# Optimization experiments

Hardware: AMD Instinct MI355X
Metric: run time of the kernel (lower is better)

The kernel has to match this reference:

```python
import jax, jax.numpy as jnp
import numpy as np

N_NODES = 50000
N_EDGES = 800000
NODE_DIM = 256
EDGE_DIM = 64
NUM_REL = 4
HID = 512      # hidden_dims[0]
LAST = 128     # last_dim_size
BATCH = 16384
EPS = 1e-10    # torchdrug RelationalGraphConv degree-normalization eps


def _glorot(k, shape):
    fan_in = shape[-1]
    return jax.random.normal(k, shape, jnp.float32) / np.sqrt(fan_in).astype(np.float32)


def setup_inputs() -> dict:
    key = jax.random.key(0)
    ks = jax.random.split(key, 20)
    inp = {}
    inp["inputs"] = jax.random.randint(ks[0], (BATCH, 3), 0, N_NODES, dtype=jnp.int32)
    inp["node_feature"] = jax.random.normal(ks[1], (N_NODES, NODE_DIM), jnp.float32)
    inp["edge_feature"] = jax.random.normal(ks[2], (N_EDGES, EDGE_DIM), jnp.float32)
    inp["edge_src"] = jax.random.randint(ks[3], (N_EDGES,), 0, N_NODES, dtype=jnp.int32)
    inp["edge_dst"] = jax.random.randint(ks[4], (N_EDGES,), 0, N_NODES, dtype=jnp.int32)
    inp["edge_rel"] = jax.random.randint(ks[5], (N_EDGES,), 0, NUM_REL, dtype=jnp.int32)
    # RGCN layer 1: 256 -> 512
    inp["We1"] = _glorot(ks[6], (NODE_DIM, EDGE_DIM)); inp["be1"] = jnp.zeros((NODE_DIM,), jnp.float32)
    inp["Wl1"] = _glorot(ks[7], (HID, NUM_REL * NODE_DIM)); inp["bl1"] = jnp.zeros((HID,), jnp.float32)
    inp["Ws1"] = _glorot(ks[8], (HID, NODE_DIM)); inp["bs1"] = jnp.zeros((HID,), jnp.float32)
    # RGCN layer 2: 512 -> 128
    inp["We2"] = _glorot(ks[9], (HID, EDGE_DIM)); inp["be2"] = jnp.zeros((HID,), jnp.float32)
    inp["Wl2"] = _glorot(ks[10], (LAST, NUM_REL * HID)); inp["bl2"] = jnp.zeros((LAST,), jnp.float32)
    inp["Ws2"] = _glorot(ks[11], (LAST, HID)); inp["bs2"] = jnp.zeros((LAST,), jnp.float32)
    # ccle_mlp: edge_dim -> 256 -> 128
    inp["Wc1"] = _glorot(ks[12], (256, EDGE_DIM)); inp["bc1"] = jnp.zeros((256,), jnp.float32)
    inp["Wc2"] = _glorot(ks[13], (LAST, 256)); inp["bc2"] = jnp.zeros((LAST,), jnp.float32)
    # final MLP: 3*128 -> 128 -> 64 -> 1
    inp["Wf1"] = _glorot(ks[14], (128, 3 * LAST)); inp["bf1"] = jnp.zeros((128,), jnp.float32)
    inp["Wf2"] = _glorot(ks[15], (64, 128)); inp["bf2"] = jnp.zeros((64,), jnp.float32)
    inp["Wf3"] = _glorot(ks[16], (1, 64)); inp["bf3"] = jnp.zeros((1,), jnp.float32)
    return inp


def _rgcn_layer(x, edge_src, edge_dst, edge_rel, edge_feat, We, be, Wl, bl, Ws, bs):
    """torchdrug RelationalGraphConv: message = x[src] + edge_linear(edge_feat);
    per-(node,relation) mean aggregation; combine = linear(update) + self_loop(x); relu."""
    in_dim = x.shape[1]
    msg = x[edge_src] + edge_feat @ We.T + be                      # [E, in_dim]
    seg = edge_dst * NUM_REL + edge_rel                            # [E]
    agg = jax.ops.segment_sum(msg, seg, num_segments=N_NODES * NUM_REL)
    cnt = jax.ops.segment_sum(jnp.ones((msg.shape[0], 1), msg.dtype), seg,
                              num_segments=N_NODES * NUM_REL)
    upd = (agg / (cnt + EPS)).reshape(N_NODES, NUM_REL * in_dim)   # [N, R*in_dim]
    return jax.nn.relu(upd @ Wl.T + bl + x @ Ws.T + bs)


def reference(inputs, node_feature, edge_feature, edge_src, edge_dst, edge_rel,
              We1, be1, Wl1, bl1, Ws1, bs1,
              We2, be2, Wl2, bl2, Ws2, bs2,
              Wc1, bc1, Wc2, bc2,
              Wf1, bf1, Wf2, bf2, Wf3, bf3):
    d1, d2, ctx = inputs[:, 0], inputs[:, 1], inputs[:, 2]
    h = _rgcn_layer(node_feature, edge_src, edge_dst, edge_rel, edge_feature,
                    We1, be1, Wl1, bl1, Ws1, bs1)
    h = _rgcn_layer(h, edge_src, edge_dst, edge_rel, edge_feature,
                    We2, be2, Wl2, bl2, Ws2, bs2)
    x1 = h[d1]                                                     # [B, 128]
    x2 = h[d2]                                                     # [B, 128]
    ef = edge_feature[ctx]                                         # [B, 64]
    x3 = jax.nn.relu(ef @ Wc1.T + bc1) @ Wc2.T + bc2               # [B, 128]
    x = jnp.concatenate([x1, x2, x3], axis=1)                      # [B, 384]
    x = jax.nn.relu(x @ Wf1.T + bf1)
    x = jax.nn.relu(x @ Wf2.T + bf2)
    return x @ Wf3.T + bf3                                         # [B, 1]
```

## Files before the change

### kernel.cpp

```cpp
#include <hip/hip_runtime.h>
#include <hip/hip_bf16.h>

#define N_NODES 50000
#define N_EDGES 800000
#define NODE_DIM 256
#define EDGE_DIM 64
#define NUM_REL 4
#define HID 512
#define LAST 128
#define BATCH 16384
#define EPS 1e-10f
#define NSEG (N_NODES * NUM_REL)

#define K1 1600
#define K2 832

typedef __bf16 bf16_t;
typedef __attribute__((ext_vector_type(8))) __bf16 bf16x8;
typedef __attribute__((ext_vector_type(4))) __bf16 bf16x4;
typedef __attribute__((ext_vector_type(2))) __bf16 bf16x2;
typedef __attribute__((ext_vector_type(4))) float f32x4;

typedef __attribute__((address_space(1))) const unsigned int g_u32;
typedef __attribute__((address_space(3))) unsigned int l_u32;
static __device__ __forceinline__ void gload16(const void* g, void* l) {
    __builtin_amdgcn_global_load_lds((g_u32*)g, (l_u32*)l, 16, 0, 0);
}

__global__ __launch_bounds__(256) void hist_kernel(
    const int* __restrict__ edst, const int* __restrict__ erel, int* __restrict__ hist)
{
    int e = blockIdx.x * 256 + threadIdx.x;
    if (e >= N_EDGES) return;
    atomicAdd(&hist[edst[e] * NUM_REL + erel[e]], 1);
}

#define SCAN_B 2048
__global__ __launch_bounds__(256) void scan1(
    const int* __restrict__ in, int* __restrict__ out, int* __restrict__ bsum, int n)
{
    __shared__ int sh[256];
    int base = blockIdx.x * SCAN_B + threadIdx.x * 8;
    int v[8]; int s = 0;
#pragma unroll
    for (int i = 0; i < 8; ++i) {
        int idx = base + i;
        v[i] = s;
        s += (idx < n) ? in[idx] : 0;
    }
    sh[threadIdx.x] = s;
    __syncthreads();
    for (int off = 1; off < 256; off <<= 1) {
        int t = (threadIdx.x >= off) ? sh[threadIdx.x - off] : 0;
        __syncthreads();
        sh[threadIdx.x] += t;
        __syncthreads();
    }
    int texcl = (threadIdx.x == 0) ? 0 : sh[threadIdx.x - 1];
#pragma unroll
    for (int i = 0; i < 8; ++i) {
        int idx = base + i;
        if (idx < n) out[idx] = texcl + v[i];
    }
    if (threadIdx.x == 255) bsum[blockIdx.x] = sh[255];
}

__global__ void scan2(int* bsum, int nb)
{
    if (threadIdx.x == 0 && blockIdx.x == 0) {
        int s = 0;
        for (int i = 0; i < nb; ++i) { int t = bsum[i]; bsum[i] = s; s += t; }
    }
}

__global__ __launch_bounds__(256) void scan3(int* __restrict__ out, const int* __restrict__ bsum, int n)
{
    int idx = blockIdx.x * SCAN_B + threadIdx.x * 8;
    int add = bsum[blockIdx.x];
#pragma unroll
    for (int i = 0; i < 8; ++i)
        if (idx + i < n) out[idx + i] += add;
}

__global__ __launch_bounds__(256) void csr_fill(
    const int* __restrict__ edst, const int* __restrict__ erel, const int* __restrict__ esrc,
    const int* __restrict__ offs, int* __restrict__ cursor,
    int* __restrict__ csr_src, int* __restrict__ csr_eid)
{
    int e = blockIdx.x * 256 + threadIdx.x;
    if (e >= N_EDGES) return;
    int seg = edst[e] * NUM_REL + erel[e];
    int pos = offs[seg] + atomicAdd(&cursor[seg], 1);
    csr_src[pos] = esrc[e];
    csr_eid[pos] = e;
}

__global__ __launch_bounds__(256) void prep_small(
    const float* __restrict__ Wc1, const float* __restrict__ Wc2,
    const float* __restrict__ Wf1, const float* __restrict__ Wf2,
    const float* __restrict__ bl1, const float* __restrict__ bs1,
    const float* __restrict__ bl2, const float* __restrict__ bs2,
    bf16_t* __restrict__ Wc1b, bf16_t* __restrict__ Wc2b,
    bf16_t* __restrict__ Wf1b, bf16_t* __restrict__ Wf2b,
    float* __restrict__ bias12, float* __restrict__ bias22)
{
    int i = blockIdx.x * 256 + threadIdx.x;
    const float* src; bf16_t* dst; int base;
    if (i < 4096)        { src = Wc1; dst = Wc1b; base = 0; }
    else if (i < 12288)  { src = Wc2; dst = Wc2b; base = 4096; }
    else if (i < 24576)  { src = Wf1; dst = Wf1b; base = 12288; }
    else if (i < 26624)  { src = Wf2; dst = Wf2b; base = 24576; }
    else {
        int j = i - 26624;
        if (j < 512) bias12[j] = bl1[j] + bs1[j];
        else if (j < 640) bias22[j - 512] = bl2[j - 512] + bs2[j - 512];
        return;
    }
    int k = i - base;
    float4 v = ((const float4*)src)[k];
    bf16x4 o;
    o[0] = (bf16_t)v.x; o[1] = (bf16_t)v.y; o[2] = (bf16_t)v.z; o[3] = (bf16_t)v.w;
    ((bf16x4*)dst)[k] = o;
}

__global__ __launch_bounds__(256) void xconv_k(const float* __restrict__ x, bf16_t* __restrict__ A1,
                                               bf16_t* __restrict__ xb)
{
    int i = blockIdx.x * 256 + threadIdx.x;
    int n = i >> 6;
    int c4 = i & 63;
    float4 v = ((const float4*)(x + (size_t)n * 256))[c4];
    bf16x4 o;
    o[0] = (bf16_t)v.x; o[1] = (bf16_t)v.y; o[2] = (bf16_t)v.z; o[3] = (bf16_t)v.w;
    *(bf16x4*)(A1 + (size_t)n * K1 + 1280 + c4 * 4) = o;
    *(bf16x4*)(xb + (size_t)n * 256 + c4 * 4) = o;
}

__global__ __launch_bounds__(256) void prep_w1cat(
    const float* __restrict__ Wl1, const float* __restrict__ We1,
    const float* __restrict__ Ws1, const float* __restrict__ be1, bf16_t* __restrict__ W1cat)
{
    int j = blockIdx.x;
    int t = threadIdx.x;
    const float* wrow = Wl1 + (size_t)j * 1024;
    bf16_t* out = W1cat + (size_t)j * K1;
    for (int c = t; c < 1024; c += 256) out[c] = (bf16_t)wrow[c];
    {
        int r = t >> 6, e = t & 63;
        float s = 0.f;
        const float* wr = wrow + r * 256;
        for (int c = 0; c < 256; ++c) s += wr[c] * We1[c * 64 + e];
        out[1024 + t] = (bf16_t)s;
    }
    if (t < 256) out[1280 + t] = (bf16_t)Ws1[(size_t)j * 256 + t];
    if (t < 4) {
        float s = 0.f;
        const float* wr = wrow + t * 256;
        for (int c = 0; c < 256; ++c) s += wr[c] * be1[c];
        out[1536 + t] = (bf16_t)s;
    }
    if (t >= 4 && t < 64) out[1536 + t] = (bf16_t)0.f;
}

__global__ __launch_bounds__(256) void prep_w2cat(
    const float* __restrict__ Wl2, const float* __restrict__ We2,
    const float* __restrict__ Ws2, const float* __restrict__ be2, bf16_t* __restrict__ W2cat)
{
    int j = blockIdx.x;
    int t = threadIdx.x;
    const float* wrow = Wl2 + (size_t)j * 2048;
    bf16_t* out = W2cat + (size_t)j * K2;
    {
        int r = t >> 6, e = t & 63;
        float s = 0.f;
        const float* wr = wrow + r * 512;
        for (int k = 0; k < 512; ++k) s += wr[k] * We2[k * 64 + e];
        out[t] = (bf16_t)s;
    }
    for (int c = t; c < 512; c += 256) out[256 + c] = (bf16_t)Ws2[(size_t)j * 512 + c];
    if (t < 4) {
        float s = 0.f;
        const float* wr = wrow + t * 512;
        for (int k = 0; k < 512; ++k) s += wr[k] * be2[k];
        out[768 + t] = (bf16_t)s;
    }
    if (t >= 4 && t < 64) out[768 + t] = (bf16_t)0.f;
}

__global__ __launch_bounds__(256) void prep_w2p(const float* __restrict__ Wl2, bf16_t* __restrict__ W2p)
{
    int idx = blockIdx.x * 256 + threadIdx.x;
    int row = idx >> 9, k = idx & 511;
    int j = row & 127, r = row >> 7;
    W2p[idx] = (bf16_t)Wl2[(size_t)j * 2048 + r * 512 + k];
}

__global__ __launch_bounds__(256) void agg1(
    const float* __restrict__ ef, const bf16_t* __restrict__ xb,
    const int* __restrict__ csr_src, const int* __restrict__ csr_eid,
    const int* __restrict__ offs, const int* __restrict__ hist,
    bf16_t* __restrict__ A1, bf16_t* __restrict__ A2)
{
    int n = blockIdx.x;
    int w = threadIdx.x >> 6;
    int lane = threadIdx.x & 63;
    int half = lane >> 5;
    int l32 = lane & 31;
    int seg = n * NUM_REL + w;
    int beg = offs[seg], ct = hist[seg];

    float xs[8] = {0.f, 0.f, 0.f, 0.f, 0.f, 0.f, 0.f, 0.f};
    float es0 = 0.f, es1 = 0.f;

    int i = 0;
    for (; i + 4 <= ct; i += 4) {
        int sA = csr_src[beg + i + half];
        int sB = csr_src[beg + i + 2 + half];
        int eA = csr_eid[beg + i + half];
        int eB = csr_eid[beg + i + 2 + half];
        bf16x8 vA = *(const bf16x8*)(xb + (size_t)sA * 256 + l32 * 8);
        bf16x8 vB = *(const bf16x8*)(xb + (size_t)sB * 256 + l32 * 8);
        float2 fA = *(const float2*)(ef + (size_t)eA * 64 + l32 * 2);
        float2 fB = *(const float2*)(ef + (size_t)eB * 64 + l32 * 2);
#pragma unroll
        for (int j = 0; j < 8; ++j) xs[j] += (float)vA[j] + (float)vB[j];
        es0 += fA.x + fB.x;
        es1 += fA.y + fB.y;
    }
    for (; i + 2 <= ct; i += 2) {
        int sA = csr_src[beg + i + half];
        int eA = csr_eid[beg + i + half];
        bf16x8 vA = *(const bf16x8*)(xb + (size_t)sA * 256 + l32 * 8);
        float2 fA = *(const float2*)(ef + (size_t)eA * 64 + l32 * 2);
#pragma unroll
        for (int j = 0; j < 8; ++j) xs[j] += (float)vA[j];
        es0 += fA.x;
        es1 += fA.y;
    }
    if (i < ct && half == 0) {
        int sA = csr_src[beg + i];
        int eA = csr_eid[beg + i];
        bf16x8 vA = *(const bf16x8*)(xb + (size_t)sA * 256 + l32 * 8);
        float2 fA = *(const float2*)(ef + (size_t)eA * 64 + l32 * 2);
#pragma unroll
        for (int j = 0; j < 8; ++j) xs[j] += (float)vA[j];
        es0 += fA.x;
        es1 += fA.y;
    }
#pragma unroll
    for (int j = 0; j < 8; ++j) xs[j] += __shfl_xor(xs[j], 32);
    es0 += __shfl_xor(es0, 32);
    es1 += __shfl_xor(es1, 32);

    float inv = 1.0f / ((float)ct + EPS);
    if (half == 0) {
        bf16x8 m;
#pragma unroll
        for (int j = 0; j < 8; ++j) m[j] = (bf16_t)(xs[j] * inv);
        *(bf16x8*)(A1 + (size_t)n * K1 + w * 256 + l32 * 8) = m;
        bf16x2 e2;
        e2[0] = (bf16_t)(es0 * inv);
        e2[1] = (bf16_t)(es1 * inv);
        *(bf16x2*)(A1 + (size_t)n * K1 + 1024 + w * 64 + l32 * 2) = e2;
        *(bf16x2*)(A2 + (size_t)n * K2 + w * 64 + l32 * 2) = e2;
    }
    if (lane == 0) {
        bf16_t fv = (bf16_t)((float)ct * inv);
        A1[(size_t)n * K1 + 1536 + w] = fv;
        A2[(size_t)n * K2 + 768 + w] = fv;
    }
    if (w == 3 && lane >= 4) {
        A1[(size_t)n * K1 + 1536 + lane] = (bf16_t)0.f;
        A2[(size_t)n * K2 + 768 + lane] = (bf16_t)0.f;
    }
}

__global__ __launch_bounds__(256) void agg2(
    const bf16_t* __restrict__ P, const int* __restrict__ csr_src,
    const int* __restrict__ offs, const int* __restrict__ hist,
    float* __restrict__ h2base)
{
    __shared__ float red[4][128];
    int n = blockIdx.x;
    int w = threadIdx.x >> 6;
    int lane = threadIdx.x & 63;
    int half = lane >> 5;
    int l32 = lane & 31;
    int seg = n * NUM_REL + w;
    int beg = offs[seg], ct = hist[seg];

    float s0 = 0.f, s1 = 0.f, s2 = 0.f, s3 = 0.f;
    int i = 0;
    for (; i + 4 <= ct; i += 4) {
        int a = csr_src[beg + i + half];
        int b = csr_src[beg + i + 2 + half];
        bf16x4 va = *(const bf16x4*)(P + (size_t)a * HID + w * 128 + l32 * 4);
        bf16x4 vb = *(const bf16x4*)(P + (size_t)b * HID + w * 128 + l32 * 4);
        s0 += (float)va[0] + (float)vb[0];
        s1 += (float)va[1] + (float)vb[1];
        s2 += (float)va[2] + (float)vb[2];
        s3 += (float)va[3] + (float)vb[3];
    }
    for (; i + 2 <= ct; i += 2) {
        int a = csr_src[beg + i + half];
        bf16x4 va = *(const bf16x4*)(P + (size_t)a * HID + w * 128 + l32 * 4);
        s0 += (float)va[0]; s1 += (float)va[1]; s2 += (float)va[2]; s3 += (float)va[3];
    }
    if (i < ct && half == 0) {
        int a = csr_src[beg + i];
        bf16x4 va = *(const bf16x4*)(P + (size_t)a * HID + w * 128 + l32 * 4);
        s0 += (float)va[0]; s1 += (float)va[1]; s2 += (float)va[2]; s3 += (float)va[3];
    }
    s0 += __shfl_xor(s0, 32);
    s1 += __shfl_xor(s1, 32);
    s2 += __shfl_xor(s2, 32);
    s3 += __shfl_xor(s3, 32);

    float inv = 1.0f / ((float)ct + EPS);
    if (half == 0) {
        red[w][l32 * 4 + 0] = s0 * inv;
        red[w][l32 * 4 + 1] = s1 * inv;
        red[w][l32 * 4 + 2] = s2 * inv;
        red[w][l32 * 4 + 3] = s3 * inv;
    }
    __syncthreads();
    int t = threadIdx.x;
    if (t < 128)
        h2base[(size_t)n * 128 + t] = red[0][t] + red[1][t] + red[2][t] + red[3][t];
}

template<int RELU, int ACC, int OUTBF>
__global__ __launch_bounds__(256) void gemm_bf16(
    const bf16_t* __restrict__ A, int lda,
    const bf16_t* __restrict__ W, int ldw,
    const float* __restrict__ Cin, int ldcin,
    const float* __restrict__ bias,
    void* __restrict__ Cout, int ldc,
    int M, int N, int K, int ncol)
{
    __shared__ char smem[65536];
    const int tid = threadIdx.x;

    const int nwg = gridDim.x;
    const int q8 = nwg >> 3, r8 = nwg & 7;
    const int xcd = blockIdx.x & 7, li = blockIdx.x >> 3;
    const int wgid = (xcd < r8 ? xcd * (q8 + 1) : r8 * (q8 + 1) + (xcd - r8) * q8) + li;

    const int row0 = (wgid / ncol) * 128;
    const int col0 = (wgid % ncol) * 128;
    const int lane = tid & 63, wv = tid >> 6;

    const int rsub = lane >> 3;
    const int gchunk = (lane & 7) ^ rsub;
    const bf16_t* pa[4]; const bf16_t* pb[4];
    int lofs[4];
#pragma unroll
    for (int s = 0; s < 4; ++s) {
        int q = wv * 4 + s;
        int ar = row0 + q * 8 + rsub; if (ar >= M) ar = M - 1;
        int br = col0 + q * 8 + rsub; if (br >= N) br = N - 1;
        pa[s] = A + (size_t)ar * lda + gchunk * 8;
        pb[s] = W + (size_t)br * ldw + gchunk * 8;
        lofs[s] = q * 1024;
    }

    const int wm = wv >> 1, wn = wv & 1;
    const int r16 = lane & 15, kch = lane >> 4;
    const int sw = r16 & 7;

    f32x4 acc[4][4];
#pragma unroll
    for (int i = 0; i < 4; ++i)
#pragma unroll
        for (int j = 0; j < 4; ++j) acc[i][j] = (f32x4){0.f, 0.f, 0.f, 0.f};

#pragma unroll
    for (int s = 0; s < 4; ++s) {
        gload16(pa[s], smem + lofs[s]);
        gload16(pb[s], smem + 16384 + lofs[s]);
    }

    const int nk = K >> 6;
    int cur = 0;
    for (int it = 0; it < nk; ++it) {
        const int k0 = it << 6;
        if (it + 1 < nk) {
            char* nb = smem + ((cur ^ 1) << 15);
#pragma unroll
            for (int s = 0; s < 4; ++s) {
                gload16(pa[s] + k0 + 64, nb + lofs[s]);
                gload16(pb[s] + k0 + 64, nb + 16384 + lofs[s]);
            }
            asm volatile("s_waitcnt vmcnt(8)" ::: "memory");
        } else {
            asm volatile("s_waitcnt vmcnt(0)" ::: "memory");
        }
        __builtin_amdgcn_s_barrier();
        __builtin_amdgcn_sched_barrier(0);
        const char* As = smem + (cur << 15);
        const char* Bs = As + 16384;
#pragma unroll
        for (int t = 0; t < 2; ++t) {
            const int slot = ((t * 4 + kch) ^ sw) << 4;
            bf16x8 af[4], bfm[4];
#pragma unroll
            for (int i = 0; i < 4; ++i)
                af[i] = *(const bf16x8*)(As + (wm * 64 + i * 16 + r16) * 128 + slot);
#pragma unroll
            for (int j = 0; j < 4; ++j)
                bfm[j] = *(const bf16x8*)(Bs + (wn * 64 + j * 16 + r16) * 128 + slot);
#pragma unroll
            for (int i = 0; i < 4; ++i)
#pragma unroll
                for (int j = 0; j < 4; ++j)
                    acc[i][j] = __builtin_amdgcn_mfma_f32_16x16x32_bf16(af[i], bfm[j], acc[i][j], 0, 0, 0);
        }
        __builtin_amdgcn_s_barrier();
        cur ^= 1;
    }

    const int crow0 = row0 + wm * 64;
#pragma unroll
    for (int i = 0; i < 4; ++i) {
#pragma unroll
        for (int j = 0; j < 4; ++j) {
            int col = col0 + wn * 64 + j * 16 + r16;
            if (col >= N) continue;
            float bv = bias ? bias[col] : 0.f;
#pragma unroll
            for (int q = 0; q < 4; ++q) {
                int row = crow0 + i * 16 + kch * 4 + q;
                if (row >= M) continue;
                float v = acc[i][j][q] + bv;
                if (ACC) v += Cin[(size_t)row * ldcin + col];
                if (RELU) v = fmaxf(v, 0.f);
                if (OUTBF) ((bf16_t*)Cout)[(size_t)row * ldc + col] = (bf16_t)v;
                else       ((float*)Cout)[(size_t)row * ldc + col] = v;
            }
        }
    }
}

__global__ __launch_bounds__(256) void gather_head(
    const int* __restrict__ inputs, const bf16_t* __restrict__ h2,
    const float* __restrict__ ef, bf16_t* __restrict__ xcat, bf16_t* __restrict__ ef_g)
{
    int i = blockIdx.x;
    int t = threadIdx.x;
    int d1 = inputs[i * 3 + 0];
    int d2 = inputs[i * 3 + 1];
    int ctx = inputs[i * 3 + 2];
    if (t < 128) {
        xcat[(size_t)i * 384 + t] = h2[(size_t)d1 * LAST + t];
    } else {
        int c = t - 128;
        xcat[(size_t)i * 384 + 128 + c] = h2[(size_t)d2 * LAST + c];
    }
    if (t < 64) ef_g[(size_t)i * 64 + t] = (bf16_t)ef[(size_t)ctx * EDGE_DIM + t];
}

__global__ __launch_bounds__(256) void final_matvec(
    const bf16_t* __restrict__ f2, const float* __restrict__ Wf3,
    const float* __restrict__ bf3, float* __restrict__ out, int M)
{
    int row = blockIdx.x * 4 + (threadIdx.x >> 6);
    int lane = threadIdx.x & 63;
    if (row >= M) return;
    float v = (float)f2[(size_t)row * 64 + lane] * Wf3[lane];
#pragma unroll
    for (int off = 32; off > 0; off >>= 1) v += __shfl_down(v, off);
    if (lane == 0) out[row] = v + bf3[0];
}

extern "C" void kernel_launch(void* const* d_in, const int* in_sizes, int n_in,
                              void* d_out, int out_size, void* d_ws, size_t ws_size,
                              hipStream_t stream)
{
    const int*   inputs       = (const int*)  d_in[0];
    const float* node_feature = (const float*)d_in[1];
    const float* edge_feature = (const float*)d_in[2];
    const int*   edge_src     = (const int*)  d_in[3];
    const int*   edge_dst     = (const int*)  d_in[4];
    const int*   edge_rel     = (const int*)  d_in[5];
    const float* We1 = (const float*)d_in[6];
    const float* be1 = (const float*)d_in[7];
    const float* Wl1 = (const float*)d_in[8];
    const float* bl1 = (const float*)d_in[9];
    const float* Ws1 = (const float*)d_in[10];
    const float* bs1 = (const float*)d_in[11];
    const float* We2 = (const float*)d_in[12];
    const float* be2 = (const float*)d_in[13];
    const float* Wl2 = (const float*)d_in[14];
    const float* bl2 = (const float*)d_in[15];
    const float* Ws2 = (const float*)d_in[16];
    const float* bs2 = (const float*)d_in[17];
    const float* Wc1 = (const float*)d_in[18];
    const float* bc1 = (const float*)d_in[19];
    const float* Wc2 = (const float*)d_in[20];
    const float* bc2 = (const float*)d_in[21];
    const float* Wf1 = (const float*)d_in[22];
    const float* bf1 = (const float*)d_in[23];
    const float* Wf2 = (const float*)d_in[24];
    const float* bf2 = (const float*)d_in[25];
    const float* Wf3 = (const float*)d_in[26];
    const float* bf3 = (const float*)d_in[27];
    float* out = (float*)d_out;

    char* p = (char*)d_ws;
    auto alloc = [&](size_t bytes) { char* r = p; p += (bytes + 255) & ~(size_t)255; return r; };
    int* hist     = (int*)alloc(NSEG * 4);
    int* offs     = (int*)alloc(NSEG * 4);
    int* cursor   = (int*)alloc(NSEG * 4);
    int* csr_src  = (int*)alloc(N_EDGES * 4);
    int* csr_eid  = (int*)alloc(N_EDGES * 4);
    int* bsums    = (int*)alloc(128 * 4);
    bf16_t* A1    = (bf16_t*)alloc((size_t)N_NODES * K1 * 2);
    bf16_t* A2    = (bf16_t*)alloc((size_t)N_NODES * K2 * 2);
    bf16_t* xb    = (bf16_t*)alloc((size_t)N_NODES * 256 * 2);
    bf16_t* Pbuf  = (bf16_t*)alloc((size_t)N_NODES * HID * 2);
    float*  h2base= (float*)alloc((size_t)N_NODES * 128 * 4);
    bf16_t* h2    = (bf16_t*)alloc((size_t)N_NODES * 128 * 2);
    bf16_t* W1cat = (bf16_t*)alloc((size_t)512 * K1 * 2);
    bf16_t* W2cat = (bf16_t*)alloc((size_t)128 * K2 * 2);
    bf16_t* W2p   = (bf16_t*)alloc((size_t)512 * 512 * 2);
    bf16_t* Wc1b  = (bf16_t*)alloc(256 * 64 * 2);
    bf16_t* Wc2b  = (bf16_t*)alloc(128 * 256 * 2);
    bf16_t* Wf1b  = (bf16_t*)alloc(128 * 384 * 2);
    bf16_t* Wf2b  = (bf16_t*)alloc(64 * 128 * 2);
    float*  bias12= (float*)alloc(512 * 4);
    float*  bias22= (float*)alloc(128 * 4);
    bf16_t* ef_g  = (bf16_t*)alloc((size_t)BATCH * 64 * 2);
    bf16_t* u3    = (bf16_t*)alloc((size_t)BATCH * 256 * 2);
    bf16_t* xcat  = (bf16_t*)alloc((size_t)BATCH * 384 * 2);
    bf16_t* f1    = (bf16_t*)alloc((size_t)BATCH * 128 * 2);
    bf16_t* f2    = (bf16_t*)alloc((size_t)BATCH * 64 * 2);

    hipMemsetAsync(hist, 0, NSEG * 4, stream);
    hipMemsetAsync(cursor, 0, NSEG * 4, stream);
    hist_kernel<<<(N_EDGES + 255) / 256, 256, 0, stream>>>(edge_dst, edge_rel, hist);
    int nscan = (NSEG + SCAN_B - 1) / SCAN_B;
    scan1<<<nscan, 256, 0, stream>>>(hist, offs, bsums, NSEG);
    scan2<<<1, 64, 0, stream>>>(bsums, nscan);
    scan3<<<nscan, 256, 0, stream>>>(offs, bsums, NSEG);
    csr_fill<<<(N_EDGES + 255) / 256, 256, 0, stream>>>(edge_dst, edge_rel, edge_src,
                                                        offs, cursor, csr_src, csr_eid);

    prep_w1cat<<<512, 256, 0, stream>>>(Wl1, We1, Ws1, be1, W1cat);
    prep_w2cat<<<128, 256, 0, stream>>>(Wl2, We2, Ws2, be2, W2cat);
    prep_w2p<<<(512 * 512) / 256, 256, 0, stream>>>(Wl2, W2p);
    prep_small<<<(26624 + 640 + 255) / 256, 256, 0, stream>>>(
        Wc1, Wc2, Wf1, Wf2, bl1, bs1, bl2, bs2,
        Wc1b, Wc2b, Wf1b, Wf2b, bias12, bias22);
    xconv_k<<<(N_NODES * 64 + 255) / 256, 256, 0, stream>>>(node_feature, A1, xb);

    agg1<<<N_NODES, 256, 0, stream>>>(edge_feature, xb, csr_src, csr_eid, offs, hist, A1, A2);
    {
        int nrow = (N_NODES + 127) / 128, ncol = HID / 128;
        gemm_bf16<1, 0, 1><<<nrow * ncol, 256, 0, stream>>>(A1, K1, W1cat, K1, nullptr, 0, bias12,
                                                            A2 + 256, K2, N_NODES, HID, K1, ncol);
    }

    {
        int nrow = (N_NODES + 127) / 128, ncol = HID / 128;
        gemm_bf16<0, 0, 1><<<nrow * ncol, 256, 0, stream>>>(A2 + 256, K2, W2p, 512, nullptr, 0, nullptr,
                                                            Pbuf, HID, N_NODES, HID, 512, ncol);
    }
    agg2<<<N_NODES, 256, 0, stream>>>(Pbuf, csr_src, offs, hist, h2base);
    {
        int nrow = (N_NODES + 127) / 128;
        gemm_bf16<1, 1, 1><<<nrow, 256, 0, stream>>>(A2, K2, W2cat, K2, h2base, 128, bias22,
                                                     h2, 128, N_NODES, 128, K2, 1);
    }

    gather_head<<<BATCH, 256, 0, stream>>>(inputs, h2, edge_feature, xcat, ef_g);
    {
        gemm_bf16<1, 0, 1><<<(BATCH / 128) * 2, 256, 0, stream>>>(ef_g, 64, Wc1b, 64, nullptr, 0, bc1,
                                                                  u3, 256, BATCH, 256, 64, 2);
    }
    {
        gemm_bf16<0, 0, 1><<<BATCH / 128, 256, 0, stream>>>(u3, 256, Wc2b, 256, nullptr, 0, bc2,
                                                            xcat + 256, 384, BATCH, 128, 256, 1);
    }
    {
        gemm_bf16<1, 0, 1><<<BATCH / 128, 256, 0, stream>>>(xcat, 384, Wf1b, 384, nullptr, 0, bf1,
                                                            f1, 128, BATCH, 128, 384, 1);
    }
    {
        gemm_bf16<1, 0, 1><<<BATCH / 128, 256, 0, stream>>>(f1, 128, Wf2b, 128, nullptr, 0, bf2,
                                                            f2, 64, BATCH, 64, 128, 1);
    }
    final_matvec<<<BATCH / 4, 256, 0, stream>>>(f2, Wf3, bf3, out, BATCH);
}
```

Baseline: 705.5 us.

## Fuse head gathers into Wf1 GEMM, fuse Wf2+final matvec, drop cursor memset

The h2[d1]/h2[d2] gathers now happen inside a dedicated Wf1 GEMM kernel that loads rows by index straight into shared memory, so the concatenated xcat buffer is no longer materialized. The Wf2 GEMM and the final dot product are merged into one head_tail kernel. The edge-feature gather is vectorized. The scan also seeds the CSR cursor with offsets, which removes a memset and one load per edge in csr_fill. Together these cut launches and intermediate traffic in the small head stages, which are a minor share of total runtime.

```diff
diff --git a/kernel.cpp b/kernel.cpp
--- a/kernel.cpp
+++ b/kernel.cpp
@@ -73,24 +73,29 @@
     }
 }
 
-__global__ __launch_bounds__(256) void scan3(int* __restrict__ out, const int* __restrict__ bsum, int n)
+__global__ __launch_bounds__(256) void scan3(int* __restrict__ out, int* __restrict__ cursor,
+                                             const int* __restrict__ bsum, int n)
 {
     int idx = blockIdx.x * SCAN_B + threadIdx.x * 8;
     int add = bsum[blockIdx.x];
 #pragma unroll
     for (int i = 0; i < 8; ++i)
-        if (idx + i < n) out[idx + i] += add;
+        if (idx + i < n) {
+            int v = out[idx + i] + add;
+            out[idx + i] = v;
+            cursor[idx + i] = v;
+        }
 }
 
 __global__ __launch_bounds__(256) void csr_fill(
     const int* __restrict__ edst, const int* __restrict__ erel, const int* __restrict__ esrc,
-    const int* __restrict__ offs, int* __restrict__ cursor,
+    int* __restrict__ cursor,
     int* __restrict__ csr_src, int* __restrict__ csr_eid)
 {
     int e = blockIdx.x * 256 + threadIdx.x;
     if (e >= N_EDGES) return;
     int seg = edst[e] * NUM_REL + erel[e];
-    int pos = offs[seg] + atomicAdd(&cursor[seg], 1);
+    int pos = atomicAdd(&cursor[seg], 1);
     csr_src[pos] = esrc[e];
     csr_eid[pos] = e;
 }
@@ -441,35 +446,159 @@
     }
 }
 
-__global__ __launch_bounds__(256) void gather_head(
+__global__ __launch_bounds__(256) void gemm_f1g(
     const int* __restrict__ inputs, const bf16_t* __restrict__ h2,
-    const float* __restrict__ ef, bf16_t* __restrict__ xcat, bf16_t* __restrict__ ef_g)
-{
-    int i = blockIdx.x;
-    int t = threadIdx.x;
-    int d1 = inputs[i * 3 + 0];
-    int d2 = inputs[i * 3 + 1];
-    int ctx = inputs[i * 3 + 2];
-    if (t < 128) {
-        xcat[(size_t)i * 384 + t] = h2[(size_t)d1 * LAST + t];
-    } else {
-        int c = t - 128;
-        xcat[(size_t)i * 384 + 128 + c] = h2[(size_t)d2 * LAST + c];
-    }
-    if (t < 64) ef_g[(size_t)i * 64 + t] = (bf16_t)ef[(size_t)ctx * EDGE_DIM + t];
-}
-
-__global__ __launch_bounds__(256) void final_matvec(
-    const bf16_t* __restrict__ f2, const float* __restrict__ Wf3,
-    const float* __restrict__ bf3, float* __restrict__ out, int M)
-{
-    int row = blockIdx.x * 4 + (threadIdx.x >> 6);
-    int lane = threadIdx.x & 63;
-    if (row >= M) return;
-    float v = (float)f2[(size_t)row * 64 + lane] * Wf3[lane];
-#pragma unroll
-    for (int off = 32; off > 0; off >>= 1) v += __shfl_down(v, off);
-    if (lane == 0) out[row] = v + bf3[0];
+    const bf16_t* __restrict__ x3, const bf16_t* __restrict__ Wf1b,
+    const float* __restrict__ bf1, bf16_t* __restrict__ f1)
+{
+    __shared__ char smem[65536];
+    const int tid = threadIdx.x;
+    const int nwg = gridDim.x;
+    const int q8 = nwg >> 3;
+    const int xcd = blockIdx.x & 7, li = blockIdx.x >> 3;
+    const int wgid = xcd * q8 + li;
+    const int row0 = wgid * 128;
+    const int lane = tid & 63, wv = tid >> 6;
+
+    const int rsub = lane >> 3;
+    const int gchunk = (lane & 7) ^ rsub;
+    const bf16_t* baseA[4][3];
+    const bf16_t* pb[4];
+    int lofs[4];
+#pragma unroll
+    for (int s = 0; s < 4; ++s) {
+        int q = wv * 4 + s;
+        int ar = row0 + q * 8 + rsub;
+        int d1 = inputs[ar * 3 + 0];
+        int d2 = inputs[ar * 3 + 1];
+        baseA[s][0] = h2 + (size_t)d1 * 128 + gchunk * 8;
+        baseA[s][1] = h2 + (size_t)d2 * 128 + gchunk * 8;
+        baseA[s][2] = x3 + (size_t)ar * 128 + gchunk * 8;
+        int br = q * 8 + rsub;
+        pb[s] = Wf1b + (size_t)br * 384 + gchunk * 8;
+        lofs[s] = q * 1024;
+    }
+
+    const int wm = wv >> 1, wn = wv & 1;
+    const int r16 = lane & 15, kch = lane >> 4;
+    const int sw = r16 & 7;
+
+    f32x4 acc[4][4];
+#pragma unroll
+    for (int i = 0; i < 4; ++i)
+#pragma unroll
+        for (int j = 0; j < 4; ++j) acc[i][j] = (f32x4){0.f, 0.f, 0.f, 0.f};
+
+#pragma unroll
+    for (int s = 0; s < 4; ++s) {
+        gload16(baseA[s][0], smem + lofs[s]);
+        gload16(pb[s], smem + 16384 + lofs[s]);
+    }
+
+    int cur = 0;
+#pragma unroll
+    for (int it = 0; it < 6; ++it) {
+        const int k0 = it << 6;
+        if (it < 5) {
+            const int kn = k0 + 64;
+            const int reg = kn >> 7, off = kn & 127;
+            char* nb = smem + ((cur ^ 1) << 15);
+#pragma unroll
+            for (int s = 0; s < 4; ++s) {
+                gload16(baseA[s][reg] + off, nb + lofs[s]);
+                gload16(pb[s] + kn, nb + 16384 + lofs[s]);
+            }
+            asm volatile("s_waitcnt vmcnt(8)" ::: "memory");
+        } else {
+            asm volatile("s_waitcnt vmcnt(0)" ::: "memory");
+        }
+        __builtin_amdgcn_s_barrier();
+        __builtin_amdgcn_sched_barrier(0);
+        const char* As = smem + (cur << 15);
+        const char* Bs = As + 16384;
+#pragma unroll
+        for (int t = 0; t < 2; ++t) {
+            const int slot = ((t * 4 + kch) ^ sw) << 4;
+            bf16x8 af[4], bfm[4];
+#pragma unroll
+            for (int i = 0; i < 4; ++i)
+                af[i] = *(const bf16x8*)(As + (wm * 64 + i * 16 + r16) * 128 + slot);
+#pragma unroll
+            for (int j = 0; j < 4; ++j)
+                bfm[j] = *(const bf16x8*)(Bs + (wn * 64 + j * 16 + r16) * 128 + slot);
+#pragma unroll
+            for (int i = 0; i < 4; ++i)
+#pragma unroll
+                for (int j = 0; j < 4; ++j)
+                    acc[i][j] = __builtin_amdgcn_mfma_f32_16x16x32_bf16(af[i], bfm[j], acc[i][j], 0, 0, 0);
+        }
+        __builtin_amdgcn_s_barrier();
+        cur ^= 1;
+    }
+
+    const int crow0 = row0 + wm * 64;
+#pragma unroll
+    for (int i = 0; i < 4; ++i) {
+#pragma unroll
+        for (int j = 0; j < 4; ++j) {
+            int col = wn * 64 + j * 16 + r16;
+            if (col >= 128) continue;
+            float bv = bf1[col];
+#pragma unroll
+            for (int q = 0; q < 4; ++q) {
+                int row = crow0 + i * 16 + kch * 4 + q;
+                float v = fmaxf(acc[i][j][q] + bv, 0.f);
+                f1[(size_t)row * 128 + col] = (bf16_t)v;
+            }
+        }
+    }
+}
+
+__global__ __launch_bounds__(256) void gather_ef(
+    const int* __restrict__ inputs, const float* __restrict__ ef, bf16_t* __restrict__ ef_g)
+{
+    int i = blockIdx.x * 256 + threadIdx.x;
+    int row = i >> 4, c4 = i & 15;
+    int ctx = inputs[row * 3 + 2];
+    float4 v = *(const float4*)(ef + (size_t)ctx * 64 + c4 * 4);
+    bf16x4 o;
+    o[0] = (bf16_t)v.x; o[1] = (bf16_t)v.y; o[2] = (bf16_t)v.z; o[3] = (bf16_t)v.w;
+    *(bf16x4*)(ef_g + (size_t)row * 64 + c4 * 4) = o;
+}
+
+__global__ __launch_bounds__(256) void head_tail(
+    const bf16_t* __restrict__ f1, const bf16_t* __restrict__ Wf2b,
+    const float* __restrict__ bf2, const float* __restrict__ Wf3,
+    const float* __restrict__ bf3, float* __restrict__ out)
+{
+    __shared__ bf16_t sf1[128 * 128];
+    int blk = blockIdx.x;
+    int tid = threadIdx.x;
+    const bf16_t* gsrc = f1 + (size_t)blk * 128 * 128;
+    for (int i = tid; i < 128 * 16; i += 256)
+        ((bf16x8*)sf1)[i] = ((const bf16x8*)gsrc)[i];
+    int lane = tid & 63, wv = tid >> 6;
+    bf16x8 w[16];
+#pragma unroll
+    for (int c = 0; c < 16; ++c) w[c] = ((const bf16x8*)(Wf2b + lane * 128))[c];
+    float bias2 = bf2[lane];
+    float wf3 = Wf3[lane];
+    float b3 = bf3[0];
+    __syncthreads();
+    for (int r = wv; r < 128; r += 4) {
+        const bf16x8* frow = (const bf16x8*)(sf1 + r * 128);
+        float acc = 0.f;
+#pragma unroll
+        for (int c = 0; c < 16; ++c) {
+            bf16x8 fv = frow[c];
+#pragma unroll
+            for (int j = 0; j < 8; ++j) acc += (float)fv[j] * (float)w[c][j];
+        }
+        float v = fmaxf(acc + bias2, 0.f) * wf3;
+#pragma unroll
+        for (int off = 32; off > 0; off >>= 1) v += __shfl_down(v, off);
+        if (lane == 0) out[blk * 128 + r] = v + b3;
+    }
 }
 
 extern "C" void kernel_launch(void* const* d_in, const int* in_sizes, int n_in,
@@ -531,19 +660,17 @@
     float*  bias22= (float*)alloc(128 * 4);
     bf16_t* ef_g  = (bf16_t*)alloc((size_t)BATCH * 64 * 2);
     bf16_t* u3    = (bf16_t*)alloc((size_t)BATCH * 256 * 2);
-    bf16_t* xcat  = (bf16_t*)alloc((size_t)BATCH * 384 * 2);
+    bf16_t* x3buf = (bf16_t*)alloc((size_t)BATCH * 128 * 2);
     bf16_t* f1    = (bf16_t*)alloc((size_t)BATCH * 128 * 2);
-    bf16_t* f2    = (bf16_t*)alloc((size_t)BATCH * 64 * 2);
 
     hipMemsetAsync(hist, 0, NSEG * 4, stream);
-    hipMemsetAsync(cursor, 0, NSEG * 4, stream);
     hist_kernel<<<(N_EDGES + 255) / 256, 256, 0, stream>>>(edge_dst, edge_rel, hist);
     int nscan = (NSEG + SCAN_B - 1) / SCAN_B;
     scan1<<<nscan, 256, 0, stream>>>(hist, offs, bsums, NSEG);
     scan2<<<1, 64, 0, stream>>>(bsums, nscan);
-    scan3<<<nscan, 256, 0, stream>>>(offs, bsums, NSEG);
+    scan3<<<nscan, 256, 0, stream>>>(offs, cursor, bsums, NSEG);
     csr_fill<<<(N_EDGES + 255) / 256, 256, 0, stream>>>(edge_dst, edge_rel, edge_src,
-                                                        offs, cursor, csr_src, csr_eid);
+                                                        cursor, csr_src, csr_eid);
 
     prep_w1cat<<<512, 256, 0, stream>>>(Wl1, We1, Ws1, be1, W1cat);
     prep_w2cat<<<128, 256, 0, stream>>>(Wl2, We2, Ws2, be2, W2cat);
@@ -572,22 +699,15 @@
                                                      h2, 128, N_NODES, 128, K2, 1);
     }
 
-    gather_head<<<BATCH, 256, 0, stream>>>(inputs, h2, edge_feature, xcat, ef_g);
+    gather_ef<<<(BATCH * 16) / 256, 256, 0, stream>>>(inputs, edge_feature, ef_g);
     {
         gemm_bf16<1, 0, 1><<<(BATCH / 128) * 2, 256, 0, stream>>>(ef_g, 64, Wc1b, 64, nullptr, 0, bc1,
                                                                   u3, 256, BATCH, 256, 64, 2);
     }
     {
         gemm_bf16<0, 0, 1><<<BATCH / 128, 256, 0, stream>>>(u3, 256, Wc2b, 256, nullptr, 0, bc2,
-                                                            xcat + 256, 384, BATCH, 128, 256, 1);
-    }
-    {
-        gemm_bf16<1, 0, 1><<<BATCH / 128, 256, 0, stream>>>(xcat, 384, Wf1b, 384, nullptr, 0, bf1,
-                                                            f1, 128, BATCH, 128, 384, 1);
-    }
-    {
-        gemm_bf16<1, 0, 1><<<BATCH / 128, 256, 0, stream>>>(f1, 128, Wf2b, 128, nullptr, 0, bf2,
-                                                            f2, 64, BATCH, 64, 128, 1);
-    }
-    final_matvec<<<BATCH / 4, 256, 0, stream>>>(f2, Wf3, bf3, out, BATCH);
-}
+                                                            x3buf, 128, BATCH, 128, 256, 1);
+    }
+    gemm_f1g<<<BATCH / 128, 256, 0, stream>>>(inputs, h2, x3buf, Wf1b, bf1, f1);
+    head_tail<<<BATCH / 128, 256, 0, stream>>>(f1, Wf2b, bf2, Wf3, bf3, out);
+}
```

Measured after the change: 694.0 us. No clear change (-1.6%).
